# Performance work log

Measured on AMD Instinct MI355X. Metric: run time of the kernel, lower is better.

## Reference

```python
import jax, jax.numpy as jnp
import numpy as np

ALPHA = 1.5
N_ITER = 50
DIM = -1


def setup_inputs() -> dict:
    key = jax.random.key(0)
    X = jax.random.normal(key, (8, 2048, 4096), dtype=jnp.float32)
    return {"X": X}


def reference(X):
    d = X.shape[DIM]
    alpha = jnp.asarray(ALPHA, X.dtype)
    Xs = (alpha - 1) * X
    m = jnp.max(Xs, axis=DIM, keepdims=True)
    t_min = m - 1
    t_max = m - jnp.asarray(d ** (1 - ALPHA), X.dtype)
    diff = t_max - t_min
    p = 1.0 / (d - 1)  # NOTE: source uses 1/(shape[dim]-1), reproduced faithfully

    def zfun(t):
        u = jnp.maximum(Xs - t, 0)
        u_safe = jnp.where(u > 0, u, 1.0)  # avoid nan grads of pow at 0
        return jnp.where(u > 0, u_safe ** p, 0.0)

    def body(carry, _):
        t_min, diff, _ = carry
        diff = diff / 2
        t = t_min + diff
        Z = zfun(t)
        mask = (jnp.sum(Z, axis=DIM, keepdims=True) - 1) >= 0
        t_min = jnp.where(mask, t, t_min)
        return (t_min, diff, t), None

    (t_min, diff, t), _ = jax.lax.scan(body, (t_min, diff, t_min), None, length=N_ITER)
    Z = zfun(t)  # Z from the final iteration's threshold t
    return Z / jnp.sum(Z, axis=DIM, keepdims=True)
```

## Files before the change

kernel.cpp:

```cpp
#include <hip/hip_runtime.h>
#include <math.h>


static constexpr int D = 4096;
static constexpr int NT = 256;
static constexpr float P = (float)(1.0 / 4095.0);

__device__ __forceinline__ float pow_p(float u) {
#if __has_builtin(__builtin_amdgcn_exp2f) && __has_builtin(__builtin_amdgcn_logf)
    return __builtin_amdgcn_exp2f(P * __builtin_amdgcn_logf(u));
#else
    return exp2f(P * log2f(u));
#endif
}

__device__ __forceinline__ float wave_sum(float v) {
#pragma unroll
    for (int k = 32; k >= 1; k >>= 1) v += __shfl_xor(v, k, 64);
    return v;
}

__device__ __forceinline__ float wave_max(float v) {
#pragma unroll
    for (int k = 32; k >= 1; k >>= 1) v = fmaxf(v, __shfl_xor(v, k, 64));
    return v;
}

__global__ void __launch_bounds__(NT) entmax_bisect_kernel(
        const float* __restrict__ X, float* __restrict__ out) {
    __shared__ float s_vals[D];
    __shared__ float s_red[4];
    __shared__ int   s_cnt;
    __shared__ float s_t, s_rsum;

    const int tid  = threadIdx.x;
    const int lane = tid & 63;
    const int wid  = tid >> 6;
    const size_t rowbase = (size_t)blockIdx.x * D;
    const float4* Xv = (const float4*)(X + rowbase);
    float4*       Ov = (float4*)(out + rowbase);

    float4 xs[4];
#pragma unroll
    for (int c = 0; c < 4; ++c) {
        float4 v = Xv[c * NT + tid];
        xs[c].x = 0.5f * v.x; xs[c].y = 0.5f * v.y;
        xs[c].z = 0.5f * v.z; xs[c].w = 0.5f * v.w;
    }

    float lmax = -3.4e38f;
#pragma unroll
    for (int c = 0; c < 4; ++c)
        lmax = fmaxf(lmax, fmaxf(fmaxf(xs[c].x, xs[c].y), fmaxf(xs[c].z, xs[c].w)));
    lmax = wave_max(lmax);
    if (tid == 0) s_cnt = 0;
    if (lane == 0) s_red[wid] = lmax;
    __syncthreads();
    const float m = fmaxf(fmaxf(s_red[0], s_red[1]), fmaxf(s_red[2], s_red[3]));
    const float tmin0 = m - 1.0f;

    int c_local = 0;
#pragma unroll
    for (int c = 0; c < 4; ++c) {
        c_local += (xs[c].x > tmin0) + (xs[c].y > tmin0)
                 + (xs[c].z > tmin0) + (xs[c].w > tmin0);
    }
    int incl = c_local;
#pragma unroll
    for (int d = 1; d < 64; d <<= 1) {
        int o = __shfl_up(incl, d, 64);
        if (lane >= d) incl += o;
    }
    int wbase = 0;
    if (lane == 63) wbase = atomicAdd(&s_cnt, incl);
    wbase = __shfl(wbase, 63, 64);
    int off = wbase + incl - c_local;
#pragma unroll
    for (int c = 0; c < 4; ++c) {
        if (xs[c].x > tmin0) s_vals[off++] = xs[c].x;
        if (xs[c].y > tmin0) s_vals[off++] = xs[c].y;
        if (xs[c].z > tmin0) s_vals[off++] = xs[c].z;
        if (xs[c].w > tmin0) s_vals[off++] = xs[c].w;
    }
    __syncthreads();

    if (wid == 0) {
        const int cnt = s_cnt;
        float t_min = tmin0;
        float diff  = (m - 0.015625f) - t_min;
        float t     = t_min;
#pragma unroll 1
        for (int it = 0; it < 50; ++it) {
            diff *= 0.5f;
            t = t_min + diff;
            if (t == t_min) break;
            float local = 0.0f;
            for (int i = lane; i < cnt; i += 64) {
                float u = s_vals[i] - t;
                if (u > 0.0f) local += pow_p(u);
            }
            float s = wave_sum(local);
            if (s - 1.0f >= 0.0f) t_min = t;
        }
        float local = 0.0f;
        for (int i = lane; i < cnt; i += 64) {
            float u = s_vals[i] - t;
            if (u > 0.0f) local += pow_p(u);
        }
        float s = wave_sum(local);
        if (lane == 0) { s_t = t; s_rsum = 1.0f / s; }
    }
    __syncthreads();
    const float tf = s_t, rsum = s_rsum;

#pragma unroll
    for (int c = 0; c < 4; ++c) {
        float4 o; float u;
        u = xs[c].x - tf; o.x = (u > 0.0f) ? pow_p(u) * rsum : 0.0f;
        u = xs[c].y - tf; o.y = (u > 0.0f) ? pow_p(u) * rsum : 0.0f;
        u = xs[c].z - tf; o.z = (u > 0.0f) ? pow_p(u) * rsum : 0.0f;
        u = xs[c].w - tf; o.w = (u > 0.0f) ? pow_p(u) * rsum : 0.0f;
        Ov[c * NT + tid] = o;
    }
}

extern "C" void kernel_launch(void* const* d_in, const int* in_sizes, int n_in,
                              void* d_out, int out_size, void* d_ws, size_t ws_size,
                              hipStream_t stream) {
    const float* X = (const float*)d_in[0];
    float* O = (float*)d_out;
    const int nrows = in_sizes[0] / D;
    hipLaunchKernelGGL(entmax_bisect_kernel, dim3(nrows), dim3(NT), 0, stream, X, O);
}
```

Baseline: 456.5 us.

## Replace bisection sum evaluations with top-2 threshold comparison

With p = 1/4095 and every shifted value at most 1 above the initial lower bound, each positive term u^p is close to 1 but never exceeds 1. The bisection test 'sum >= 1' therefore reduces to 'at least two elements exceed t', which is the same as t < second-largest value. The kernel now computes a block-wide top-2 and runs the 50-step bisection as scalar arithmetic in every thread. This removes the shared-memory compaction, the atomic-based prefix scan and the per-iteration pow/sum passes. It relies on the analytic property of this exponent and dimension and can diverge slightly from the reference's float summation in edge cases.

```diff
diff --git a/kernel.cpp b/kernel.cpp
--- a/kernel.cpp
+++ b/kernel.cpp
@@ -20,18 +20,15 @@
     return v;
 }
 
-__device__ __forceinline__ float wave_max(float v) {
-#pragma unroll
-    for (int k = 32; k >= 1; k >>= 1) v = fmaxf(v, __shfl_xor(v, k, 64));
-    return v;
+__device__ __forceinline__ void top2_merge(float& hi, float& lo, float ohi, float olo) {
+    float nhi = fmaxf(hi, ohi);
+    float nlo = fmaxf(fminf(hi, ohi), fmaxf(lo, olo));
+    hi = nhi; lo = nlo;
 }
 
 __global__ void __launch_bounds__(NT) entmax_bisect_kernel(
         const float* __restrict__ X, float* __restrict__ out) {
-    __shared__ float s_vals[D];
-    __shared__ float s_red[4];
-    __shared__ int   s_cnt;
-    __shared__ float s_t, s_rsum;
+    __shared__ float s_hi[4], s_lo[4], s_sum[4];
 
     const int tid  = threadIdx.x;
     const int lane = tid & 63;
@@ -48,78 +45,62 @@
         xs[c].z = 0.5f * v.z; xs[c].w = 0.5f * v.w;
     }
 
-    float lmax = -3.4e38f;
-#pragma unroll
-    for (int c = 0; c < 4; ++c)
-        lmax = fmaxf(lmax, fmaxf(fmaxf(xs[c].x, xs[c].y), fmaxf(xs[c].z, xs[c].w)));
-    lmax = wave_max(lmax);
-    if (tid == 0) s_cnt = 0;
-    if (lane == 0) s_red[wid] = lmax;
-    __syncthreads();
-    const float m = fmaxf(fmaxf(s_red[0], s_red[1]), fmaxf(s_red[2], s_red[3]));
-    const float tmin0 = m - 1.0f;
-
-    int c_local = 0;
+    float hi = -3.4e38f, lo = -3.4e38f;
 #pragma unroll
     for (int c = 0; c < 4; ++c) {
-        c_local += (xs[c].x > tmin0) + (xs[c].y > tmin0)
-                 + (xs[c].z > tmin0) + (xs[c].w > tmin0);
+        const float vv[4] = {xs[c].x, xs[c].y, xs[c].z, xs[c].w};
+#pragma unroll
+        for (int j = 0; j < 4; ++j) {
+            float v = vv[j];
+            if (v > hi) { lo = hi; hi = v; }
+            else        { lo = fmaxf(lo, v); }
+        }
     }
-    int incl = c_local;
 #pragma unroll
-    for (int d = 1; d < 64; d <<= 1) {
-        int o = __shfl_up(incl, d, 64);
-        if (lane >= d) incl += o;
+    for (int k = 32; k >= 1; k >>= 1) {
+        float ohi = __shfl_xor(hi, k, 64);
+        float olo = __shfl_xor(lo, k, 64);
+        top2_merge(hi, lo, ohi, olo);
     }
-    int wbase = 0;
-    if (lane == 63) wbase = atomicAdd(&s_cnt, incl);
-    wbase = __shfl(wbase, 63, 64);
-    int off = wbase + incl - c_local;
+    if (lane == 0) { s_hi[wid] = hi; s_lo[wid] = lo; }
+    __syncthreads();
+    float m = s_hi[0], s2 = s_lo[0];
+#pragma unroll
+    for (int w = 1; w < 4; ++w) top2_merge(m, s2, s_hi[w], s_lo[w]);
+
+    float t_min = m - 1.0f;
+    float diff  = (m - 0.015625f) - t_min;
+    float t     = t_min;
+#pragma unroll 1
+    for (int it = 0; it < 50; ++it) {
+        diff *= 0.5f;
+        t = t_min + diff;
+        if (t == t_min) break;
+        if (t < s2) t_min = t;
+    }
+
+    float local = 0.0f;
 #pragma unroll
     for (int c = 0; c < 4; ++c) {
-        if (xs[c].x > tmin0) s_vals[off++] = xs[c].x;
-        if (xs[c].y > tmin0) s_vals[off++] = xs[c].y;
-        if (xs[c].z > tmin0) s_vals[off++] = xs[c].z;
-        if (xs[c].w > tmin0) s_vals[off++] = xs[c].w;
-    }
-    __syncthreads();
-
-    if (wid == 0) {
-        const int cnt = s_cnt;
-        float t_min = tmin0;
-        float diff  = (m - 0.015625f) - t_min;
-        float t     = t_min;
-#pragma unroll 1
-        for (int it = 0; it < 50; ++it) {
-            diff *= 0.5f;
-            t = t_min + diff;
-            if (t == t_min) break;
-            float local = 0.0f;
-            for (int i = lane; i < cnt; i += 64) {
-                float u = s_vals[i] - t;
-                if (u > 0.0f) local += pow_p(u);
-            }
-            float s = wave_sum(local);
-            if (s - 1.0f >= 0.0f) t_min = t;
-        }
-        float local = 0.0f;
-        for (int i = lane; i < cnt; i += 64) {
-            float u = s_vals[i] - t;
+        const float vv[4] = {xs[c].x, xs[c].y, xs[c].z, xs[c].w};
+#pragma unroll
+        for (int j = 0; j < 4; ++j) {
+            float u = vv[j] - t;
             if (u > 0.0f) local += pow_p(u);
         }
-        float s = wave_sum(local);
-        if (lane == 0) { s_t = t; s_rsum = 1.0f / s; }
     }
+    local = wave_sum(local);
+    if (lane == 0) s_sum[wid] = local;
     __syncthreads();
-    const float tf = s_t, rsum = s_rsum;
+    const float rsum = 1.0f / (s_sum[0] + s_sum[1] + s_sum[2] + s_sum[3]);
 
 #pragma unroll
     for (int c = 0; c < 4; ++c) {
         float4 o; float u;
-        u = xs[c].x - tf; o.x = (u > 0.0f) ? pow_p(u) * rsum : 0.0f;
-        u = xs[c].y - tf; o.y = (u > 0.0f) ? pow_p(u) * rsum : 0.0f;
-        u = xs[c].z - tf; o.z = (u > 0.0f) ? pow_p(u) * rsum : 0.0f;
-        u = xs[c].w - tf; o.w = (u > 0.0f) ? pow_p(u) * rsum : 0.0f;
+        u = xs[c].x - t; o.x = (u > 0.0f) ? pow_p(u) * rsum : 0.0f;
+        u = xs[c].y - t; o.y = (u > 0.0f) ? pow_p(u) * rsum : 0.0f;
+        u = xs[c].z - t; o.z = (u > 0.0f) ? pow_p(u) * rsum : 0.0f;
+        u = xs[c].w - t; o.w = (u > 0.0f) ? pow_p(u) * rsum : 0.0f;
         Ov[c * NT + tid] = o;
     }
 }
```

Result: faster. 428.1 us (-6.2%).
